# Kernel tuning notes

Hardware: AMD Instinct MI355X
Metric: run time of the kernel (lower is better)

## Reference

```python
import jax, jax.numpy as jnp
import numpy as np

N_HEADS = 8
D_K = 64
SCALE = D_K ** -0.5


def setup_inputs() -> dict:
    key = jax.random.key(0)
    k1, k2, k3, k4, k5 = jax.random.split(key, 5)
    C = 512
    inner = N_HEADS * D_K  # 512
    return {
        "x": jax.random.normal(k1, (16, C, 32, 32), dtype=jnp.float32),
        "W_qkv": jax.random.normal(k2, (C, 3 * inner), dtype=jnp.float32) * (C ** -0.5),
        "b_qkv": jax.random.normal(k3, (3 * inner,), dtype=jnp.float32) * 0.02,
        "W_out": jax.random.normal(k4, (inner, C), dtype=jnp.float32) * (inner ** -0.5),
        "b_out": jax.random.normal(k5, (C,), dtype=jnp.float32) * 0.02,
    }


def reference(x, W_qkv, b_qkv, W_out, b_out):
    B, C, H, W = x.shape
    N = H * W
    xt = x.reshape(B, C, N).transpose(0, 2, 1)  # (B, N, C) tokens
    qkv = (xt @ W_qkv + b_qkv).reshape(B, N, N_HEADS, 3 * D_K)
    q, k, v = jnp.split(qkv, 3, axis=-1)  # each (B, N, H, d_k)
    # scores over key axis j; softmax along j (original dim=2 of bijh)
    attn = jnp.einsum('bihd,bjhd->bhij', q, k) * SCALE
    attn = jax.nn.softmax(attn, axis=-1)
    res = jnp.einsum('bhij,bjhd->bihd', attn, v).reshape(B, N, N_HEADS * D_K)
    res = res @ W_out + b_out + xt  # out projection + residual (note: GroupNorm unused in source forward)
    return res.transpose(0, 2, 1).reshape(B, C, H, W)
```

## Files before the change

kernel.cpp:

```cpp
#include <hip/hip_runtime.h>
#include <hip/hip_bf16.h>
#include <stdint.h>

#define N_HEADS 8
#define D_K 64
#define QSCALE (0.125f * 1.44269504088896f)

typedef __attribute__((ext_vector_type(4))) float f32x4;
typedef __attribute__((ext_vector_type(16))) float f32x16;
typedef __attribute__((ext_vector_type(8))) short bf16x8;
typedef __attribute__((ext_vector_type(4))) unsigned short u16x4;
typedef __attribute__((ext_vector_type(4))) unsigned int u32x4;

#define AS1 __attribute__((address_space(1)))
#define AS3 __attribute__((address_space(3)))

static __device__ __forceinline__ void gload_lds16(const void* g, void* l) {
    __builtin_amdgcn_global_load_lds((const AS1 void*)g, (AS3 void*)l, 16, 0, 0);
}

static __device__ __forceinline__ __hip_bfloat16 f2bf(float f) {
    return __float2bfloat16(f);
}

static __device__ __forceinline__ unsigned short bfbits(float f) {
    return __builtin_bit_cast(unsigned short, __float2bfloat16(f));
}

static __device__ __forceinline__ uint32_t pkbf(float lo, float hi) {
    return (uint32_t)bfbits(lo) | ((uint32_t)bfbits(hi) << 16);
}

static __device__ __forceinline__ float fexp2(float x) {
#if __has_builtin(__builtin_amdgcn_exp2f)
    return __builtin_amdgcn_exp2f(x);
#else
    float r;
    asm("v_exp_f32 %0, %1" : "=v"(r) : "v"(x));
    return r;
#endif
}

static __device__ __forceinline__ float fmax3(float a, float b, float c) {
    return fmaxf(fmaxf(a, b), c);
}

__global__ __launch_bounds__(256) void transpose_bf16(
    const float* __restrict__ in, __hip_bfloat16* __restrict__ out,
    int R, int C) {
    __shared__ float tile[32][33];
    const int bz = blockIdx.z;
    const int r0 = blockIdx.y * 32, c0 = blockIdx.x * 32;
    const float* ip = in + (size_t)bz * R * C;
    __hip_bfloat16* op = out + (size_t)bz * R * C;
    const int tx = threadIdx.x & 31, ty = threadIdx.x >> 5;
#pragma unroll
    for (int i = 0; i < 4; ++i)
        tile[ty + i * 8][tx] = ip[(size_t)(r0 + ty + i * 8) * C + c0 + tx];
    __syncthreads();
    const int c = threadIdx.x >> 3, rg = threadIdx.x & 7;
    u16x4 v;
#pragma unroll
    for (int j = 0; j < 4; ++j) v[j] = bfbits(tile[rg * 4 + j][c]);
    *(u16x4*)(op + (size_t)(c0 + c) * R + r0 + rg * 4) = v;
}

__device__ __forceinline__ void gemm128_tile(
    const __hip_bfloat16* __restrict__ Abase, int lda,
    const __hip_bfloat16* __restrict__ Bbase, int ldb,
    int K,
    __hip_bfloat16* Atile, __hip_bfloat16* Btile,
    f32x4 (&acc)[4][4]) {
    const int t = threadIdx.x;
    const int w = t >> 6;
    const int l = t & 63;
    const int wr = (w >> 1) * 64, wc = (w & 1) * 64;
    const int fr = l & 15, fq = l >> 4;

#pragma unroll
    for (int m = 0; m < 4; ++m)
#pragma unroll
        for (int n = 0; n < 4; ++n) acc[m][n] = (f32x4)0.f;

    auto stage = [&](int buf, int k0) {
#pragma unroll
        for (int i = 0; i < 2; ++i) {
            const int tt = t + i * 256;
            const int row = tt >> 2;
            const int sl = (tt & 3) ^ (row & 3);
            char* la = (char*)Atile + buf * 8192 + i * 4096 + w * 1024;
            char* lb = (char*)Btile + buf * 8192 + i * 4096 + w * 1024;
            gload_lds16(Abase + (size_t)row * lda + k0 + sl * 8, la);
            gload_lds16(Bbase + (size_t)row * ldb + k0 + sl * 8, lb);
        }
    };

    const int nkt = K >> 5;
    stage(0, 0);
    __syncthreads();

    for (int kt = 0; kt < nkt; ++kt) {
        const int cur = kt & 1;
        if (kt + 1 < nkt) stage(cur ^ 1, (kt + 1) * 32);

        const char* Ab = (const char*)Atile + cur * 8192;
        const char* Bb = (const char*)Btile + cur * 8192;
        bf16x8 af[4], bfr[4];
#pragma unroll
        for (int m = 0; m < 4; ++m) {
            const int row = wr + m * 16 + fr;
            af[m] = *(const bf16x8*)(Ab + ((row * 64 + fq * 16) ^ ((row & 3) << 4)));
        }
#pragma unroll
        for (int n = 0; n < 4; ++n) {
            const int row = wc + n * 16 + fr;
            bfr[n] = *(const bf16x8*)(Bb + ((row * 64 + fq * 16) ^ ((row & 3) << 4)));
        }
#pragma unroll
        for (int m = 0; m < 4; ++m)
#pragma unroll
            for (int n = 0; n < 4; ++n)
                acc[m][n] = __builtin_amdgcn_mfma_f32_16x16x32_bf16(af[m], bfr[n], acc[m][n], 0, 0, 0);

        __syncthreads();
    }
}

__global__ __launch_bounds__(256) void qkv_gemm(
    const __hip_bfloat16* __restrict__ xt,
    const __hip_bfloat16* __restrict__ Wqt,
    const float* __restrict__ bias,
    __hip_bfloat16* __restrict__ q_ws,
    __hip_bfloat16* __restrict__ k_ws,
    __hip_bfloat16* __restrict__ v_ws) {
    __shared__ __attribute__((aligned(16))) __hip_bfloat16 Atile[2][128 * 32];
    __shared__ __attribute__((aligned(16))) __hip_bfloat16 Btile[2][128 * 32];
    const int id0 = blockIdx.x;
    const int wg = (id0 & 7) * 192 + (id0 >> 3);
    const int tn = wg % 12;
    const int tm = (wg / 12) & 7;
    const int b  = wg / 96;
    f32x4 acc[4][4];
    gemm128_tile(xt + ((size_t)b * 1024 + tm * 128) * 512, 512,
                 Wqt + (size_t)tn * 128 * 512, 512, 512,
                 &Atile[0][0], &Btile[0][0], acc);

    const int t = threadIdx.x, l = t & 63, w = t >> 6;
    const int wr = (w >> 1) * 64, wc = (w & 1) * 64, fr = l & 15, fq = l >> 4;
#pragma unroll
    for (int m = 0; m < 4; ++m) {
        const int nnb = tm * 128 + wr + m * 16 + fq * 4;
#pragma unroll
        for (int n = 0; n < 4; ++n) {
            const int j = tn * 128 + wc + n * 16 + fr;
            const int h = j / 192, rem = j % 192, p = rem / 64, d = rem % 64;
            const float bj = bias[j];
            const size_t bh = (size_t)b * 8 + h;
            float vv[4];
#pragma unroll
            for (int r = 0; r < 4; ++r) vv[r] = acc[m][n][r] + bj;
            if (p == 0) {
#pragma unroll
                for (int r = 0; r < 4; ++r)
                    q_ws[(bh * 1024 + nnb + r) * 64 + d] = f2bf(vv[r] * QSCALE);
            } else if (p == 1) {
                const int base = (nnb >> 6) * 4096 + (d >> 4) * 1024 +
                                 ((nnb >> 5) & 1) * 512 + ((d >> 3) & 1) * 256 +
                                 (nnb & 31) * 8 + (d & 7);
                __hip_bfloat16* kp = k_ws + bh * 65536 + base;
#pragma unroll
                for (int r = 0; r < 4; ++r) kp[r * 8] = f2bf(vv[r]);
            } else {
                const int base = (nnb >> 6) * 4096 + ((nnb >> 4) & 3) * 1024 +
                                 (d >> 5) * 512 +
                                 (((nnb >> 3) & 1) * 32 + (d & 31)) * 8 + (nnb & 7);
                u16x4 pk;
#pragma unroll
                for (int r = 0; r < 4; ++r) pk[r] = bfbits(vv[r]);
                *(u16x4*)(v_ws + bh * 65536 + base) = pk;
            }
        }
    }
}

__global__ __launch_bounds__(256) void attn_kernel(
    const __hip_bfloat16* __restrict__ q_ws,
    const __hip_bfloat16* __restrict__ k_ws,
    const __hip_bfloat16* __restrict__ v_ws,
    __hip_bfloat16* __restrict__ ao) {
    __shared__ __attribute__((aligned(16))) __hip_bfloat16 KtS[2][4096];

    const int id = blockIdx.x;
    const int bh = id & 127;
    const int qt = id >> 7;
    const int t = threadIdx.x, l = t & 63, w = t >> 6;
    const int lq = l & 31, hi = l >> 5;
    const int qrow = qt * 128 + w * 32 + lq;

    const __hip_bfloat16* qp = q_ws + ((size_t)bh * 1024 + qrow) * 64;
    bf16x8 qb[4];
#pragma unroll
    for (int s = 0; s < 4; ++s) qb[s] = *(const bf16x8*)(qp + s * 16 + hi * 8);

    f32x16 oacc[2];
    oacc[0] = (f32x16)0.f; oacc[1] = (f32x16)0.f;
    float m = -1e30f, lsum = 0.f;

    const __hip_bfloat16* kbase = k_ws + (size_t)bh * 65536;
    const char* vbase = (const char*)(v_ws + (size_t)bh * 65536);

    auto stage = [&](int buf, int kt2) {
#pragma unroll
        for (int i = 0; i < 2; ++i) {
            const int tt = t + i * 256;
            char* kd = (char*)&KtS[buf][0] + w * 1024 + i * 4096;
            gload_lds16(kbase + (size_t)kt2 * 4096 + tt * 8, kd);
        }
    };

    stage(0, 0);
    __syncthreads();

    for (int kt = 0; kt < 16; ++kt) {
        const int cur = kt & 1;
        if (kt < 15) stage(cur ^ 1, kt + 1);

        const char* KtC = (const char*)&KtS[cur][0];

        f32x16 s0 = (f32x16)0.f, s1 = (f32x16)0.f;
        __builtin_amdgcn_s_setprio(1);
#pragma unroll
        for (int s = 0; s < 4; ++s) {
            bf16x8 k0 = *(const bf16x8*)(KtC + s * 2048 + l * 16);
            bf16x8 k1 = *(const bf16x8*)(KtC + s * 2048 + 1024 + l * 16);
            s0 = __builtin_amdgcn_mfma_f32_32x32x16_bf16(k0, qb[s], s0, 0, 0, 0);
            s1 = __builtin_amdgcn_mfma_f32_32x32x16_bf16(k1, qb[s], s1, 0, 0, 0);
        }
        __builtin_amdgcn_s_setprio(0);

        const char* vpc = vbase + (size_t)kt * 8192;
        bf16x8 vf0[4], vf1[4];
#pragma unroll
        for (int s = 0; s < 4; ++s) {
            vf0[s] = *(const bf16x8*)(vpc + s * 2048 + l * 16);
            vf1[s] = *(const bf16x8*)(vpc + s * 2048 + 1024 + l * 16);
        }

        float c0 = fmax3(s0[0], s0[1], s0[2]);
        float c1 = fmax3(s0[4], s0[5], s0[6]);
        float c2 = fmax3(s0[8], s0[9], s0[10]);
        float c3 = fmax3(s0[12], s0[13], s0[14]);
        c0 = fmax3(c0, s0[3], s1[0]);
        c1 = fmax3(c1, s0[7], s1[4]);
        c2 = fmax3(c2, s0[11], s1[8]);
        c3 = fmax3(c3, s0[15], s1[12]);
        c0 = fmax3(c0, s1[1], s1[2]);
        c1 = fmax3(c1, s1[5], s1[6]);
        c2 = fmax3(c2, s1[9], s1[10]);
        c3 = fmax3(c3, s1[13], s1[14]);
        c0 = fmax3(c0, s1[3], c1);
        c2 = fmax3(c2, s1[7], s1[11]);
        float pmax = fmax3(c0, c2, fmaxf(c3, s1[15]));
        pmax = fmaxf(pmax, __shfl_xor(pmax, 32, 64));

        if (__any(pmax - m > 8.f)) {
            const float mn = fmaxf(m, pmax);
            const float corr = fexp2(m - mn);
            m = mn;
            lsum *= corr;
#pragma unroll
            for (int i = 0; i < 16; ++i) { oacc[0][i] *= corr; oacc[1][i] *= corr; }
        }

        float la0 = 0.f, la1 = 0.f, la2 = 0.f, la3 = 0.f;
#pragma unroll
        for (int i = 0; i < 16; i += 4) {
            s0[i + 0] = fexp2(s0[i + 0] - m); la0 += s0[i + 0];
            s0[i + 1] = fexp2(s0[i + 1] - m); la1 += s0[i + 1];
            s0[i + 2] = fexp2(s0[i + 2] - m); la2 += s0[i + 2];
            s0[i + 3] = fexp2(s0[i + 3] - m); la3 += s0[i + 3];
        }
#pragma unroll
        for (int i = 0; i < 16; i += 4) {
            s1[i + 0] = fexp2(s1[i + 0] - m); la0 += s1[i + 0];
            s1[i + 1] = fexp2(s1[i + 1] - m); la1 += s1[i + 1];
            s1[i + 2] = fexp2(s1[i + 2] - m); la2 += s1[i + 2];
            s1[i + 3] = fexp2(s1[i + 3] - m); la3 += s1[i + 3];
        }
        lsum += (la0 + la1) + (la2 + la3);

#pragma unroll
        for (int s = 0; s < 4; ++s) {
            const int rb = (s & 1) * 8;
            uint32_t pk01, pk23, pk45, pk67;
            if (s < 2) {
                pk01 = pkbf(s0[rb + 0], s0[rb + 1]); pk23 = pkbf(s0[rb + 2], s0[rb + 3]);
                pk45 = pkbf(s0[rb + 4], s0[rb + 5]); pk67 = pkbf(s0[rb + 6], s0[rb + 7]);
            } else {
                pk01 = pkbf(s1[rb + 0], s1[rb + 1]); pk23 = pkbf(s1[rb + 2], s1[rb + 3]);
                pk45 = pkbf(s1[rb + 4], s1[rb + 5]); pk67 = pkbf(s1[rb + 6], s1[rb + 7]);
            }
            const uint32_t sentA = hi ? pk01 : pk45;
            const uint32_t sentB = hi ? pk23 : pk67;
            const uint32_t recvA = (uint32_t)__shfl_xor((int)sentA, 32, 64);
            const uint32_t recvB = (uint32_t)__shfl_xor((int)sentB, 32, 64);
            u32x4 fw;
            fw[0] = hi ? recvA : pk01;
            fw[1] = hi ? recvB : pk23;
            fw[2] = hi ? pk45 : recvA;
            fw[3] = hi ? pk67 : recvB;
            const bf16x8 pf = __builtin_bit_cast(bf16x8, fw);

            __builtin_amdgcn_s_setprio(1);
            oacc[0] = __builtin_amdgcn_mfma_f32_32x32x16_bf16(vf0[s], pf, oacc[0], 0, 0, 0);
            oacc[1] = __builtin_amdgcn_mfma_f32_32x32x16_bf16(vf1[s], pf, oacc[1], 0, 0, 0);
            __builtin_amdgcn_s_setprio(0);
        }

        __syncthreads();
    }

    lsum += __shfl_xor(lsum, 32, 64);
    const float inv = 1.f / lsum;
    const int b = bh >> 3, h = bh & 7;
    __hip_bfloat16* aop = ao + ((size_t)b * 1024 + qrow) * 512 + h * 64;
#pragma unroll
    for (int dd = 0; dd < 2; ++dd)
#pragma unroll
        for (int rg = 0; rg < 4; ++rg) {
            u16x4 pkd;
#pragma unroll
            for (int j = 0; j < 4; ++j)
                pkd[j] = bfbits(oacc[dd][rg * 4 + j] * inv);
            const int d0 = dd * 32 + rg * 8 + hi * 4;
            *(u16x4*)(aop + d0) = pkd;
        }
}

__global__ __launch_bounds__(256) void out_gemm(
    const __hip_bfloat16* __restrict__ Wot,
    const __hip_bfloat16* __restrict__ ao,
    const float* __restrict__ bias,
    const float* __restrict__ x,
    float* __restrict__ out) {
    __shared__ __attribute__((aligned(16))) __hip_bfloat16 Atile[2][128 * 32];
    __shared__ __attribute__((aligned(16))) __hip_bfloat16 Btile[2][128 * 32];
    const int id0 = blockIdx.x;
    const int wg = (id0 & 7) * 64 + (id0 >> 3);
    const int tn = wg & 7;
    const int tc = (wg >> 3) & 3;
    const int b  = wg >> 5;
    f32x4 acc[4][4];
    gemm128_tile(Wot + (size_t)tc * 128 * 512, 512,
                 ao + ((size_t)b * 1024 + tn * 128) * 512, 512, 512,
                 &Atile[0][0], &Btile[0][0], acc);

    const int t = threadIdx.x, l = t & 63, w = t >> 6;
    const int wr = (w >> 1) * 64, wc = (w & 1) * 64, fr = l & 15, fq = l >> 4;
#pragma unroll
    for (int m = 0; m < 4; ++m) {
#pragma unroll
        for (int n = 0; n < 4; ++n) {
            const int nn = tn * 128 + wc + n * 16 + fr;
#pragma unroll
            for (int r = 0; r < 4; ++r) {
                const int c = tc * 128 + wr + m * 16 + fq * 4 + r;
                const size_t idx = ((size_t)b * 512 + c) * 1024 + nn;
                out[idx] = acc[m][n][r] + bias[c] + x[idx];
            }
        }
    }
}

extern "C" void kernel_launch(void* const* d_in, const int* in_sizes, int n_in,
                              void* d_out, int out_size, void* d_ws, size_t ws_size,
                              hipStream_t stream) {
    const float* x     = (const float*)d_in[0];
    const float* W_qkv = (const float*)d_in[1];
    const float* b_qkv = (const float*)d_in[2];
    const float* W_out = (const float*)d_in[3];
    const float* b_out = (const float*)d_in[4];
    float* out = (float*)d_out;

    const int B = 16, C = 512, N = 1024, BH = B * N_HEADS;

    char* ws = (char*)d_ws;
    __hip_bfloat16* xt   = (__hip_bfloat16*)ws; ws += (size_t)B * N * C * 2;
    __hip_bfloat16* Wqt  = (__hip_bfloat16*)ws; ws += (size_t)1536 * 512 * 2;
    __hip_bfloat16* Wot  = (__hip_bfloat16*)ws; ws += (size_t)512 * 512 * 2;
    __hip_bfloat16* q_ws = (__hip_bfloat16*)ws; ws += (size_t)BH * N * 64 * 2;
    __hip_bfloat16* k_ws = (__hip_bfloat16*)ws; ws += (size_t)BH * N * 64 * 2;
    __hip_bfloat16* v_ws = (__hip_bfloat16*)ws; ws += (size_t)BH * 64 * N * 2;
    __hip_bfloat16* ao   = (__hip_bfloat16*)ws; ws += (size_t)B * N * 512 * 2;

    transpose_bf16<<<dim3(N / 32, C / 32, B), 256, 0, stream>>>(x, xt, C, N);
    transpose_bf16<<<dim3(1536 / 32, 512 / 32, 1), 256, 0, stream>>>(W_qkv, Wqt, 512, 1536);
    transpose_bf16<<<dim3(512 / 32, 512 / 32, 1), 256, 0, stream>>>(W_out, Wot, 512, 512);

    qkv_gemm<<<dim3(1536), 256, 0, stream>>>(xt, Wqt, b_qkv, q_ws, k_ws, v_ws);

    attn_kernel<<<dim3(1024), 256, 0, stream>>>(q_ws, k_ws, v_ws, ao);

    out_gemm<<<dim3(512), 256, 0, stream>>>(Wot, ao, b_out, x, out);
}
```

Baseline: 142.1 us.

## Software-pipeline QK^T of the next key tile with softmax of the current

Restructures the attention loop so that the QK^T MFMAs for tile kt+1 are issued before the softmax and PV work of tile kt. Each tile's LDS buffer is refilled two tiles ahead. The loop is unrolled by two, ping-ponging two sets of score accumulators, and the V fragment loads move after the bf16 packing of P. The aim is to overlap matrix-core work with the exp and max VALU work and hide the latency of LDS and global loads. The cost is roughly 32 extra accumulator registers per lane, which could lower occupancy or cause spills.

```diff
diff --git a/kernel.cpp b/kernel.cpp
--- a/kernel.cpp
+++ b/kernel.cpp
@@ -218,49 +218,41 @@
         }
     };
 
-    stage(0, 0);
-    __syncthreads();
-
-    for (int kt = 0; kt < 16; ++kt) {
-        const int cur = kt & 1;
-        if (kt < 15) stage(cur ^ 1, kt + 1);
-
-        const char* KtC = (const char*)&KtS[cur][0];
-
-        f32x16 s0 = (f32x16)0.f, s1 = (f32x16)0.f;
+    auto qk = [&](const __hip_bfloat16* Kt, f32x16& o0, f32x16& o1) {
+        const char* KtC = (const char*)Kt;
+        o0 = (f32x16)0.f; o1 = (f32x16)0.f;
         __builtin_amdgcn_s_setprio(1);
 #pragma unroll
         for (int s = 0; s < 4; ++s) {
             bf16x8 k0 = *(const bf16x8*)(KtC + s * 2048 + l * 16);
             bf16x8 k1 = *(const bf16x8*)(KtC + s * 2048 + 1024 + l * 16);
-            s0 = __builtin_amdgcn_mfma_f32_32x32x16_bf16(k0, qb[s], s0, 0, 0, 0);
-            s1 = __builtin_amdgcn_mfma_f32_32x32x16_bf16(k1, qb[s], s1, 0, 0, 0);
+            o0 = __builtin_amdgcn_mfma_f32_32x32x16_bf16(k0, qb[s], o0, 0, 0, 0);
+            o1 = __builtin_amdgcn_mfma_f32_32x32x16_bf16(k1, qb[s], o1, 0, 0, 0);
         }
         __builtin_amdgcn_s_setprio(0);
-
-        const char* vpc = vbase + (size_t)kt * 8192;
-        bf16x8 vf0[4], vf1[4];
-#pragma unroll
-        for (int s = 0; s < 4; ++s) {
-            vf0[s] = *(const bf16x8*)(vpc + s * 2048 + l * 16);
-            vf1[s] = *(const bf16x8*)(vpc + s * 2048 + 1024 + l * 16);
-        }
-
-        float c0 = fmax3(s0[0], s0[1], s0[2]);
-        float c1 = fmax3(s0[4], s0[5], s0[6]);
-        float c2 = fmax3(s0[8], s0[9], s0[10]);
-        float c3 = fmax3(s0[12], s0[13], s0[14]);
-        c0 = fmax3(c0, s0[3], s1[0]);
-        c1 = fmax3(c1, s0[7], s1[4]);
-        c2 = fmax3(c2, s0[11], s1[8]);
-        c3 = fmax3(c3, s0[15], s1[12]);
-        c0 = fmax3(c0, s1[1], s1[2]);
-        c1 = fmax3(c1, s1[5], s1[6]);
-        c2 = fmax3(c2, s1[9], s1[10]);
-        c3 = fmax3(c3, s1[13], s1[14]);
-        c0 = fmax3(c0, s1[3], c1);
-        c2 = fmax3(c2, s1[7], s1[11]);
-        float pmax = fmax3(c0, c2, fmaxf(c3, s1[15]));
+    };
+
+    auto body = [&](int kt, f32x16& ca0, f32x16& ca1, f32x16& na0, f32x16& na1) {
+        const int cur = kt & 1;
+        if (kt < 14) stage(cur, kt + 2);
+
+        if (kt < 15) qk(&KtS[cur ^ 1][0], na0, na1);
+
+        float c0 = fmax3(ca0[0], ca0[1], ca0[2]);
+        float c1 = fmax3(ca0[4], ca0[5], ca0[6]);
+        float c2 = fmax3(ca0[8], ca0[9], ca0[10]);
+        float c3 = fmax3(ca0[12], ca0[13], ca0[14]);
+        c0 = fmax3(c0, ca0[3], ca1[0]);
+        c1 = fmax3(c1, ca0[7], ca1[4]);
+        c2 = fmax3(c2, ca0[11], ca1[8]);
+        c3 = fmax3(c3, ca0[15], ca1[12]);
+        c0 = fmax3(c0, ca1[1], ca1[2]);
+        c1 = fmax3(c1, ca1[5], ca1[6]);
+        c2 = fmax3(c2, ca1[9], ca1[10]);
+        c3 = fmax3(c3, ca1[13], ca1[14]);
+        c0 = fmax3(c0, ca1[3], c1);
+        c2 = fmax3(c2, ca1[7], ca1[11]);
+        float pmax = fmax3(c0, c2, fmaxf(c3, ca1[15]));
         pmax = fmaxf(pmax, __shfl_xor(pmax, 32, 64));
 
         if (__any(pmax - m > 8.f)) {
@@ -275,31 +267,49 @@
         float la0 = 0.f, la1 = 0.f, la2 = 0.f, la3 = 0.f;
 #pragma unroll
         for (int i = 0; i < 16; i += 4) {
-            s0[i + 0] = fexp2(s0[i + 0] - m); la0 += s0[i + 0];
-            s0[i + 1] = fexp2(s0[i + 1] - m); la1 += s0[i + 1];
-            s0[i + 2] = fexp2(s0[i + 2] - m); la2 += s0[i + 2];
-            s0[i + 3] = fexp2(s0[i + 3] - m); la3 += s0[i + 3];
+            ca0[i + 0] = fexp2(ca0[i + 0] - m); la0 += ca0[i + 0];
+            ca0[i + 1] = fexp2(ca0[i + 1] - m); la1 += ca0[i + 1];
+            ca0[i + 2] = fexp2(ca0[i + 2] - m); la2 += ca0[i + 2];
+            ca0[i + 3] = fexp2(ca0[i + 3] - m); la3 += ca0[i + 3];
         }
 #pragma unroll
         for (int i = 0; i < 16; i += 4) {
-            s1[i + 0] = fexp2(s1[i + 0] - m); la0 += s1[i + 0];
-            s1[i + 1] = fexp2(s1[i + 1] - m); la1 += s1[i + 1];
-            s1[i + 2] = fexp2(s1[i + 2] - m); la2 += s1[i + 2];
-            s1[i + 3] = fexp2(s1[i + 3] - m); la3 += s1[i + 3];
+            ca1[i + 0] = fexp2(ca1[i + 0] - m); la0 += ca1[i + 0];
+            ca1[i + 1] = fexp2(ca1[i + 1] - m); la1 += ca1[i + 1];
+            ca1[i + 2] = fexp2(ca1[i + 2] - m); la2 += ca1[i + 2];
+            ca1[i + 3] = fexp2(ca1[i + 3] - m); la3 += ca1[i + 3];
         }
         lsum += (la0 + la1) + (la2 + la3);
 
+        uint32_t pkw[16];
 #pragma unroll
         for (int s = 0; s < 4; ++s) {
             const int rb = (s & 1) * 8;
-            uint32_t pk01, pk23, pk45, pk67;
             if (s < 2) {
-                pk01 = pkbf(s0[rb + 0], s0[rb + 1]); pk23 = pkbf(s0[rb + 2], s0[rb + 3]);
-                pk45 = pkbf(s0[rb + 4], s0[rb + 5]); pk67 = pkbf(s0[rb + 6], s0[rb + 7]);
+                pkw[s * 4 + 0] = pkbf(ca0[rb + 0], ca0[rb + 1]);
+                pkw[s * 4 + 1] = pkbf(ca0[rb + 2], ca0[rb + 3]);
+                pkw[s * 4 + 2] = pkbf(ca0[rb + 4], ca0[rb + 5]);
+                pkw[s * 4 + 3] = pkbf(ca0[rb + 6], ca0[rb + 7]);
             } else {
-                pk01 = pkbf(s1[rb + 0], s1[rb + 1]); pk23 = pkbf(s1[rb + 2], s1[rb + 3]);
-                pk45 = pkbf(s1[rb + 4], s1[rb + 5]); pk67 = pkbf(s1[rb + 6], s1[rb + 7]);
+                pkw[s * 4 + 0] = pkbf(ca1[rb + 0], ca1[rb + 1]);
+                pkw[s * 4 + 1] = pkbf(ca1[rb + 2], ca1[rb + 3]);
+                pkw[s * 4 + 2] = pkbf(ca1[rb + 4], ca1[rb + 5]);
+                pkw[s * 4 + 3] = pkbf(ca1[rb + 6], ca1[rb + 7]);
             }
+        }
+
+        const char* vpc = vbase + (size_t)kt * 8192;
+        bf16x8 vf0[4], vf1[4];
+#pragma unroll
+        for (int s = 0; s < 4; ++s) {
+            vf0[s] = *(const bf16x8*)(vpc + s * 2048 + l * 16);
+            vf1[s] = *(const bf16x8*)(vpc + s * 2048 + 1024 + l * 16);
+        }
+
+#pragma unroll
+        for (int s = 0; s < 4; ++s) {
+            const uint32_t pk01 = pkw[s * 4 + 0], pk23 = pkw[s * 4 + 1];
+            const uint32_t pk45 = pkw[s * 4 + 2], pk67 = pkw[s * 4 + 3];
             const uint32_t sentA = hi ? pk01 : pk45;
             const uint32_t sentB = hi ? pk23 : pk67;
             const uint32_t recvA = (uint32_t)__shfl_xor((int)sentA, 32, 64);
@@ -318,6 +328,18 @@
         }
 
         __syncthreads();
+    };
+
+    stage(0, 0);
+    __syncthreads();
+    f32x16 a0, a1, b0, b1;
+    qk(&KtS[0][0], a0, a1);
+    stage(1, 1);
+    __syncthreads();
+
+    for (int it = 0; it < 8; ++it) {
+        body(2 * it,     a0, a1, b0, b1);
+        body(2 * it + 1, b0, b1, a0, a1);
     }
 
     lsum += __shfl_xor(lsum, 32, 64);
```

New measurement: 145.3 us. 1.02x slower.
